# Optimization experiments

Measured on AMD Instinct MI355X. Metric: run time of the kernel, lower is better.

Reference implementation:

```python
import jax, jax.numpy as jnp
import numpy as np

NUM_KP = 17
EDGES = [(0,1),(1,3),(0,2),(2,4),(0,5),(5,7),(7,9),(5,11),(11,13),(13,15),(0,6),(6,8),(8,10),(6,12),(12,14),(14,16)]
NUM_EDGES = len(EDGES)
IMG_H = IMG_W = 401


def bilinear_sampler(x, v):
    # x, v: [N, H, W, 2]. Faithful port of the TF gather_nd bilinear sampler
    # (pad-by-1 border, floor/ceil corners, out-of-bounds -> index 0 into pad).
    N, H, W, C = x.shape
    xp = jnp.pad(x, ((0, 0), (1, 1), (1, 1), (0, 0)))  # zeros pad
    vx = v[..., 0]
    vy = v[..., 1]
    hgrid = jnp.arange(1, H + 1, dtype=jnp.float32)[None, :, None]  # [1,H,1]
    wgrid = jnp.arange(1, W + 1, dtype=jnp.float32)[None, None, :]  # [1,1,W]
    vx0 = jnp.floor(vx); vy0 = jnp.floor(vy)
    vx1 = jnp.ceil(vx);  vy1 = jnp.ceil(vy)
    iy0 = vy0 + hgrid; iy1 = vy1 + hgrid
    ix0 = vx0 + wgrid; ix1 = vx1 + wgrid
    Hf = jnp.float32(H); Wf = jnp.float32(W)
    mask = (ix0 < 1.0) | (iy0 < 1.0) | (ix1 > Wf) | (iy1 > Hf)
    zero = jnp.zeros_like(iy0)
    iy0 = jnp.where(mask, zero, iy0)
    iy1 = jnp.where(mask, zero, iy1)
    ix0 = jnp.where(mask, zero, ix0)
    ix1 = jnp.where(mask, zero, ix1)
    n = jnp.arange(N)[:, None, None]
    iy0i = iy0.astype(jnp.int32); iy1i = iy1.astype(jnp.int32)
    ix0i = ix0.astype(jnp.int32); ix1i = ix1.astype(jnp.int32)
    x00 = xp[n, iy0i, ix0i]  # [N,H,W,C]
    x01 = xp[n, iy1i, ix0i]
    x10 = xp[n, iy0i, ix1i]
    x11 = xp[n, iy1i, ix1i]
    dx = (vx - vx0)[..., None]
    dy = (vy - vy0)[..., None]
    w00 = (1.0 - dx) * (1.0 - dy)
    w01 = (1.0 - dx) * dy
    w10 = dx * (1.0 - dy)
    w11 = dx * dy
    return w00 * x00 + w01 * x01 + w10 * x10 + w11 * x11


def refine(base, offsets, num_steps=2):
    for _ in range(num_steps):
        base = base + bilinear_sampler(offsets, base)
    return base


def conv1x1(x, w, b):
    return jnp.einsum('nhwc,co->nhwo', x, w) + b


def resize(m):
    N, _, _, C = m.shape
    return jax.image.resize(m, (N, IMG_H, IMG_W, C), method='bilinear')


def setup_inputs() -> dict:
    key = jax.random.key(0)
    ks = jax.random.split(key, 11)
    N, H, W, Cin = 2, 13, 13, 2048
    s = 0.01
    return {
        'x': jax.random.normal(ks[0], (N, H, W, Cin), jnp.float32),
        'kp_w': jax.random.normal(ks[1], (Cin, NUM_KP), jnp.float32) * s,
        'kp_b': jax.random.normal(ks[2], (NUM_KP,), jnp.float32) * s,
        'so_w': jax.random.normal(ks[3], (Cin, 2 * NUM_KP), jnp.float32) * s,
        'so_b': jax.random.normal(ks[4], (2 * NUM_KP,), jnp.float32) * s,
        'mo_w': jax.random.normal(ks[5], (Cin, 4 * NUM_EDGES), jnp.float32) * s,
        'mo_b': jax.random.normal(ks[6], (4 * NUM_EDGES,), jnp.float32) * s,
        'lo_w': jax.random.normal(ks[7], (Cin, 2 * NUM_KP), jnp.float32) * s,
        'lo_b': jax.random.normal(ks[8], (2 * NUM_KP,), jnp.float32) * s,
        'ss_w': jax.random.normal(ks[9], (Cin, 1), jnp.float32) * s,
        'ss_b': jax.random.normal(ks[10], (1,), jnp.float32) * s,
    }


def reference(x, kp_w, kp_b, so_w, so_b, mo_w, mo_b, lo_w, lo_b, ss_w, ss_b):
    N = x.shape[0]
    kp = jax.nn.sigmoid(conv1x1(x, kp_w, kp_b))
    so = conv1x1(x, so_w, so_b)
    mo = conv1x1(x, mo_w, mo_b)
    lo = conv1x1(x, lo_w, lo_b)
    ss = jax.nn.sigmoid(conv1x1(x, ss_w, ss_b))
    kp, so, mo, lo, ss = (resize(m) for m in (kp, so, mo, lo, ss))
    # Split channels into (x,y)-offset groups: [K, N, H, W, 2]
    S = so.reshape(N, IMG_H, IMG_W, NUM_KP, 2).transpose(3, 0, 1, 2, 4)
    L = lo.reshape(N, IMG_H, IMG_W, NUM_KP, 2).transpose(3, 0, 1, 2, 4)
    # long: refine against itself, then against short offsets (2 steps each)
    Lr = jax.vmap(lambda l, s: refine(refine(l, l), s))(L, S)
    long_out = Lr.transpose(1, 2, 3, 0, 4).reshape(N, IMG_H, IMG_W, 2 * NUM_KP)
    # mid: one group per directed edge, refined against the target kp short offsets
    n_mid = 2 * NUM_EDGES
    M = mo.reshape(N, IMG_H, IMG_W, n_mid, 2).transpose(3, 0, 1, 2, 4)
    to_kp = jnp.array([e[1] for e in EDGES] + [e[0] for e in EDGES], dtype=jnp.int32)
    Mr = jax.vmap(lambda m, s: refine(m, s))(M, S[to_kp])
    mid_out = Mr.transpose(1, 2, 3, 0, 4).reshape(N, IMG_H, IMG_W, 4 * NUM_EDGES)
    return (kp, so, mid_out, long_out, ss)
```

## Files before the change

kernel.cpp:

```cpp
#include <hip/hip_runtime.h>
#include <math.h>

#define IMG 401
#define NKP 17
#define NMID 32
#define CCH 150

#define OFF_KP   0ULL
#define OFF_SO   5467234ULL
#define OFF_MID  16401702ULL
#define OFF_LONG 36984230ULL
#define OFF_SS   47918698ULL

#define SCc (13.0f/401.0f)
#define C0c (13.0f/802.0f - 0.5f)

typedef float v2f __attribute__((ext_vector_type(2)));

__device__ float  g_coarse[2 * 169 * CCH];
__device__ float2 g_pairs[2 * 66 * 169];

__constant__ int TO_KP_C[32] = {1,3,2,4,5,7,9,11,13,15,6,8,10,12,14,16,
                                0,1,0,2,0,5,7,5,11,13,0,6,8,6,12,14};

__device__ __forceinline__ float med3(float a, float b, float c) {
  return __builtin_amdgcn_fmed3f(a, b, c);
}
__device__ __forceinline__ void store2(float* p, float a, float b) {
  *reinterpret_cast<float2*>(p) = make_float2(a, b);
}
__device__ __forceinline__ v2f ldb(const float2* p, int byteoff) {
  return *reinterpret_cast<const v2f*>(reinterpret_cast<const char*>(p) + byteoff);
}

__global__ __launch_bounds__(512)
void heads_kernel(const float* __restrict__ x,
                  const float* __restrict__ kp_w, const float* __restrict__ kp_b,
                  const float* __restrict__ so_w, const float* __restrict__ so_b,
                  const float* __restrict__ mo_w, const float* __restrict__ mo_b,
                  const float* __restrict__ lo_w, const float* __restrict__ lo_b,
                  const float* __restrict__ ss_w, const float* __restrict__ ss_b) {
  __shared__ float xs[2][2048];
  __shared__ float ps[2][300];
  const int p0 = blockIdx.x * 2;
  const int tid = threadIdx.x;
  const float* xr = x + (size_t)p0 * 2048;
  for (int t = tid; t < 4096; t += 512) xs[t >> 11][t & 2047] = xr[t];
  __syncthreads();
  const int part = tid / 150;
  const int c = tid - part * 150;
  float a0 = 0.f, a1 = 0.f;
  const float* bptr = nullptr; int cc = 0; bool sig = false;
  if (part < 3) {
    const float* wptr; int Ch;
    if (c < 17)       { wptr = kp_w; bptr = kp_b; Ch = 17; cc = c;       sig = true; }
    else if (c < 51)  { wptr = so_w; bptr = so_b; Ch = 34; cc = c - 17; }
    else if (c < 115) { wptr = mo_w; bptr = mo_b; Ch = 64; cc = c - 51; }
    else if (c < 149) { wptr = lo_w; bptr = lo_b; Ch = 34; cc = c - 115; }
    else              { wptr = ss_w; bptr = ss_b; Ch = 1;  cc = 0;       sig = true; }
    const float* wp = wptr + cc;
    const int k0 = part * 683, k1 = (part == 2) ? 2048 : (k0 + 683);
    #pragma unroll 8
    for (int k = k0; k < k1; ++k) {
      float wv = wp[k * Ch];
      a0 = fmaf(xs[0][k], wv, a0);
      a1 = fmaf(xs[1][k], wv, a1);
    }
    if (part) { ps[0][c + (part - 1) * 150] = a0; ps[1][c + (part - 1) * 150] = a1; }
  }
  __syncthreads();
  if (part == 0) {
    float b = bptr[cc];
    float v0 = a0 + ps[0][c] + ps[0][c + 150] + b;
    float v1 = a1 + ps[1][c] + ps[1][c + 150] + b;
    if (sig) { v0 = 1.0f / (1.0f + expf(-v0)); v1 = 1.0f / (1.0f + expf(-v1)); }
    g_coarse[(size_t)p0 * CCH + c] = v0;
    g_coarse[(size_t)(p0 + 1) * CCH + c] = v1;
    if (c >= 17 && c < 149) {
      int rel = c - 17;
      int fi = rel >> 1, lo = rel & 1;
      int nn0 = p0 / 169, pp0 = p0 - nn0 * 169;
      int nn1 = (p0 + 1) / 169, pp1 = (p0 + 1) - nn1 * 169;
      ((float*)g_pairs)[(((size_t)nn0 * 66 + fi) * 169 + pp0) * 2 + lo] = v0;
      ((float*)g_pairs)[(((size_t)nn1 * 66 + fi) * 169 + pp1) * 2 + lo] = v1;
    }
  }
}

struct Pix {
  v2f Q0, Q1;
  v2f SWH;
  v2f LOV;
  v2f HIV;
  int ob;
  int pix;
  bool valid;
};

__device__ __forceinline__ Pix mkpix(int n, int w, int h) {
  Pix P;
  P.valid = (w < IMG) && (h < IMG);
  v2f WH = {(float)w, (float)h};
  v2f S = WH * SCc + C0c;
  float cx = med3(floorf(S.x), 0.f, 11.f);
  float cy = med3(floorf(S.y), 0.f, 11.f);
  float fx = med3(S.x - cx, 0.f, 1.f);
  float fy = med3(S.y - cy, 0.f, 1.f);
  float gx = 1.f - fx, gy = 1.f - fy;
  P.Q0 = (v2f){gx, fx} * gy;
  P.Q1 = (v2f){gx, fx} * fy;
  P.ob = (int)fmaf(cy, 104.f, cx * 8.f);
  P.SWH = S;
  P.LOV = -WH;
  P.HIV = 400.f - WH;
  P.pix = (n * IMG + h) * IMG + w;
  return P;
}

__device__ __forceinline__ v2f blp4b(const float2* __restrict__ F, const Pix& P) {
  return P.Q0.x * ldb(F, P.ob)       + P.Q0.y * ldb(F, P.ob + 8)
       + P.Q1.x * ldb(F, P.ob + 104) + P.Q1.y * ldb(F, P.ob + 112);
}

__device__ __forceinline__ v2f samplePk(const float2* __restrict__ F, v2f v, const Pix& P) {
  v2f F0 = {floorf(v.x), floorf(v.y)};
  v2f D  = v - F0;
  v2f E  = {D.x > 0.f ? 1.f : 0.f, D.y > 0.f ? 1.f : 0.f};
  v2f J1 = F0 + E;
  float sel = (F0.x < P.LOV.x || F0.y < P.LOV.y ||
               J1.x > P.HIV.x || J1.y > P.HIV.y) ? 0.f : 1.f;
  v2f S0 = F0 * SCc + P.SWH;
  v2f S1 = E  * SCc + S0;
  v2f C0 = {med3(floorf(S0.x), 0.f, 11.f), med3(floorf(S0.y), 0.f, 11.f)};
  v2f C1 = {med3(floorf(S1.x), 0.f, 11.f), med3(floorf(S1.y), 0.f, 11.f)};
  v2f U0t = S0 - C0;
  v2f U0 = {med3(U0t.x, 0.f, 1.f), med3(U0t.y, 0.f, 1.f)};
  v2f U1t = S1 - C1;
  v2f U1 = {med3(U1t.x, 0.f, 1.f), med3(U1t.y, 0.f, 1.f)};
  v2f DD = C1 - C0;
  v2f G  = 1.f - D;
  v2f E0 = G * U0;
  v2f E1 = D * U1;
  v2f Fd = D - E1;
  v2f M  = Fd - Fd * DD;
  v2f W0 = (G - E0) + M;
  v2f Tt = Fd - E1;
  v2f W1 = (E0 + E1) + Tt * DD;
  v2f W2 = E1 * DD;
  int a = (int)fmaf(C0.y, 104.f, C0.x * 8.f);
  v2f r0 = W0.x*ldb(F,a)     + W1.x*ldb(F,a+8)   + W2.x*ldb(F,a+16);
  v2f r1 = W0.x*ldb(F,a+104) + W1.x*ldb(F,a+112) + W2.x*ldb(F,a+120);
  v2f r2 = W0.x*ldb(F,a+208) + W1.x*ldb(F,a+216) + W2.x*ldb(F,a+224);
  v2f acc = W0.y*r0 + W1.y*r1 + W2.y*r2;
  return acc * sel;
}

__device__ __forceinline__ void kp_item(int f, int n, int w0, int h0,
                                        const float* __restrict__ cb,
                                        float* __restrict__ out) {
  int r = f / 544, rem = f - r * 544;
  int px = rem / 17, c = rem - px * 17;
  Pix P = mkpix(n, w0 + px, h0 + r);
  if (P.valid) {
    const float* b0 = cb + (P.ob >> 3) * CCH + c;
    float v = P.Q0.x*b0[0] + P.Q0.y*b0[CCH] + P.Q1.x*b0[13*CCH] + P.Q1.y*b0[14*CCH];
    out[OFF_KP + (size_t)P.pix * 17 + c] = v;
  }
}

__device__ __forceinline__ void solong_item(int f, int n, int w0, int h0,
                                            const float2* __restrict__ Sf,
                                            const float2* __restrict__ Lf,
                                            float* __restrict__ out) {
  int r = f / 544, rem = f - r * 544;
  int px = rem / 17, k = rem - px * 17;
  Pix P = mkpix(n, w0 + px, h0 + r);
  const float2* S = Sf + k * 169;
  const float2* L = Lf + k * 169;
  v2f sv = blp4b(S, P);
  v2f b  = blp4b(L, P);
  b += samplePk(L, b, P);
  b += samplePk(L, b, P);
  b += samplePk(S, b, P);
  b += samplePk(S, b, P);
  if (P.valid) {
    store2(out + OFF_SO   + (size_t)P.pix * 34 + 2 * k, sv.x, sv.y);
    store2(out + OFF_LONG + (size_t)P.pix * 34 + 2 * k, b.x, b.y);
  }
}

__device__ __forceinline__ void mid_item(int f, int n, int w0, int h0,
                                         const float2* __restrict__ Sf,
                                         const float2* __restrict__ gmo,
                                         float* __restrict__ out) {
  int r = f >> 10, rem = f & 1023;
  int px = rem >> 5, g = rem & 31;
  Pix P = mkpix(n, w0 + px, h0 + r);
  const float2* G = gmo + g * 169;
  v2f b = blp4b(G, P);
  const float2* S = Sf + TO_KP_C[g] * 169;
  b += samplePk(S, b, P);
  b += samplePk(S, b, P);
  if (P.valid) store2(out + OFF_MID + (size_t)P.pix * 64 + 2 * g, b.x, b.y);
}

__global__ __launch_bounds__(512, 6)
void refine512_kernel(float* __restrict__ out) {
  __shared__ float2 Sf[NKP * 169 + 14];
  __shared__ float2 Lf[NKP * 169 + 14];
  const int n = blockIdx.z;
  const int tid = threadIdx.x;
  const int w0 = blockIdx.x * 32, h0 = blockIdx.y * 16;

  {
    const float2* gS = g_pairs + (size_t)n * 66 * 169;
    const float2* gL = g_pairs + ((size_t)n * 66 + 49) * 169;
    for (int t = tid; t < NKP * 169; t += 512) { Sf[t] = gS[t]; Lf[t] = gL[t]; }
    if (tid < 14) {
      Sf[NKP * 169 + tid] = make_float2(0.f, 0.f);
      Lf[NKP * 169 + tid] = make_float2(0.f, 0.f);
    }
  }
  __syncthreads();

  const float* cb = g_coarse + (size_t)n * 169 * CCH;

  #pragma unroll 1
  for (int it = 0; it < 4; ++it) {
    kp_item(it * 512 + tid, n, w0, h0, cb, out);
    kp_item((it + 4) * 512 + tid, n, w0, h0, cb, out);
    kp_item((it + 8) * 512 + tid, n, w0, h0, cb, out);
    kp_item((it + 12) * 512 + tid, n, w0, h0, cb, out);
  }
  kp_item(16 * 512 + tid, n, w0, h0, cb, out);

  {
    int r = tid >> 5, px = tid & 31;
    Pix P = mkpix(n, w0 + px, h0 + r);
    if (P.valid) {
      const float* b0 = cb + (P.ob >> 3) * CCH + 149;
      out[OFF_SS + (size_t)P.pix] =
          P.Q0.x*b0[0] + P.Q0.y*b0[CCH] + P.Q1.x*b0[13*CCH] + P.Q1.y*b0[14*CCH];
    }
  }

  #pragma unroll 1
  for (int it = 0; it < 5; ++it) {
    solong_item(it * 512 + tid, n, w0, h0, Sf, Lf, out);
    solong_item((it + 5) * 512 + tid, n, w0, h0, Sf, Lf, out);
    solong_item((it + 10) * 512 + tid, n, w0, h0, Sf, Lf, out);
  }
  solong_item(15 * 512 + tid, n, w0, h0, Sf, Lf, out);
  solong_item(16 * 512 + tid, n, w0, h0, Sf, Lf, out);

  const float2* gmo = g_pairs + ((size_t)n * 66 + 17) * 169;
  #pragma unroll 1
  for (int it = 0; it < 8; ++it) {
    mid_item(it * 512 + tid, n, w0, h0, Sf, gmo, out);
    mid_item((it + 8) * 512 + tid, n, w0, h0, Sf, gmo, out);
    mid_item((it + 16) * 512 + tid, n, w0, h0, Sf, gmo, out);
    mid_item((it + 24) * 512 + tid, n, w0, h0, Sf, gmo, out);
  }
}

extern "C" void kernel_launch(void* const* d_in, const int* in_sizes, int n_in,
                              void* d_out, int out_size, void* d_ws, size_t ws_size,
                              hipStream_t stream) {
  const float* x    = (const float*)d_in[0];
  const float* kp_w = (const float*)d_in[1];
  const float* kp_b = (const float*)d_in[2];
  const float* so_w = (const float*)d_in[3];
  const float* so_b = (const float*)d_in[4];
  const float* mo_w = (const float*)d_in[5];
  const float* mo_b = (const float*)d_in[6];
  const float* lo_w = (const float*)d_in[7];
  const float* lo_b = (const float*)d_in[8];
  const float* ss_w = (const float*)d_in[9];
  const float* ss_b = (const float*)d_in[10];
  float* out = (float*)d_out;

  heads_kernel<<<dim3(169), dim3(512), 0, stream>>>(x, kp_w, kp_b, so_w, so_b,
                                                    mo_w, mo_b, lo_w, lo_b,
                                                    ss_w, ss_b);
  refine512_kernel<<<dim3(13, 26, 2), dim3(512), 0, stream>>>(out);
}
```

Baseline: 170.2 us.

## Precompute per-column/row sampling LUTs, shrink tile to 14 rows, interleave two items

Replaces per-item pixel coordinate computation with small shared-memory lookup tables of per-column and per-row bilinear fractions and base offsets, built once per block. Changes the tile height from 16 to 14 rows, which makes the grid 29 rows of blocks and lowers how many pixels past the image edge are wasted. Processes two independent refine chains per thread iteration to expose instruction-level parallelism in the dependent sampler chain. The cost is more registers per thread and extra shared-memory reads, which can lower occupancy.

```diff
diff --git a/kernel.cpp b/kernel.cpp
--- a/kernel.cpp
+++ b/kernel.cpp
@@ -14,6 +14,7 @@
 
 #define SCc (13.0f/401.0f)
 #define C0c (13.0f/802.0f - 0.5f)
+#define ROWS 14
 
 typedef float v2f __attribute__((ext_vector_type(2)));
 
@@ -88,32 +89,25 @@
 }
 
 struct Pix {
-  v2f Q0, Q1;
-  v2f SWH;
-  v2f LOV;
-  v2f HIV;
+  v2f Q0, Q1, SWH, LOV, HIV;
   int ob;
   int pix;
   bool valid;
 };
 
-__device__ __forceinline__ Pix mkpix(int n, int w, int h) {
+__device__ __forceinline__ Pix mkpix2(const float4 lx, const float4 ly,
+                                      int pixbase, int r, int px, int wlim, int hlim) {
   Pix P;
-  P.valid = (w < IMG) && (h < IMG);
-  v2f WH = {(float)w, (float)h};
-  v2f S = WH * SCc + C0c;
-  float cx = med3(floorf(S.x), 0.f, 11.f);
-  float cy = med3(floorf(S.y), 0.f, 11.f);
-  float fx = med3(S.x - cx, 0.f, 1.f);
-  float fy = med3(S.y - cy, 0.f, 1.f);
+  float fx = lx.x, fy = ly.x;
   float gx = 1.f - fx, gy = 1.f - fy;
   P.Q0 = (v2f){gx, fx} * gy;
   P.Q1 = (v2f){gx, fx} * fy;
-  P.ob = (int)fmaf(cy, 104.f, cx * 8.f);
-  P.SWH = S;
-  P.LOV = -WH;
-  P.HIV = 400.f - WH;
-  P.pix = (n * IMG + h) * IMG + w;
+  P.ob  = (int)(lx.z + ly.z);
+  P.SWH = (v2f){lx.y, ly.y};
+  P.LOV = (v2f){-lx.w, -ly.w};
+  P.HIV = (v2f){400.f - lx.w, 400.f - ly.w};
+  P.pix = pixbase + r * IMG + px;
+  P.valid = (px < wlim) && (r < hlim);
   return P;
 }
 
@@ -155,62 +149,17 @@
   return acc * sel;
 }
 
-__device__ __forceinline__ void kp_item(int f, int n, int w0, int h0,
-                                        const float* __restrict__ cb,
-                                        float* __restrict__ out) {
-  int r = f / 544, rem = f - r * 544;
-  int px = rem / 17, c = rem - px * 17;
-  Pix P = mkpix(n, w0 + px, h0 + r);
-  if (P.valid) {
-    const float* b0 = cb + (P.ob >> 3) * CCH + c;
-    float v = P.Q0.x*b0[0] + P.Q0.y*b0[CCH] + P.Q1.x*b0[13*CCH] + P.Q1.y*b0[14*CCH];
-    out[OFF_KP + (size_t)P.pix * 17 + c] = v;
-  }
-}
-
-__device__ __forceinline__ void solong_item(int f, int n, int w0, int h0,
-                                            const float2* __restrict__ Sf,
-                                            const float2* __restrict__ Lf,
-                                            float* __restrict__ out) {
-  int r = f / 544, rem = f - r * 544;
-  int px = rem / 17, k = rem - px * 17;
-  Pix P = mkpix(n, w0 + px, h0 + r);
-  const float2* S = Sf + k * 169;
-  const float2* L = Lf + k * 169;
-  v2f sv = blp4b(S, P);
-  v2f b  = blp4b(L, P);
-  b += samplePk(L, b, P);
-  b += samplePk(L, b, P);
-  b += samplePk(S, b, P);
-  b += samplePk(S, b, P);
-  if (P.valid) {
-    store2(out + OFF_SO   + (size_t)P.pix * 34 + 2 * k, sv.x, sv.y);
-    store2(out + OFF_LONG + (size_t)P.pix * 34 + 2 * k, b.x, b.y);
-  }
-}
-
-__device__ __forceinline__ void mid_item(int f, int n, int w0, int h0,
-                                         const float2* __restrict__ Sf,
-                                         const float2* __restrict__ gmo,
-                                         float* __restrict__ out) {
-  int r = f >> 10, rem = f & 1023;
-  int px = rem >> 5, g = rem & 31;
-  Pix P = mkpix(n, w0 + px, h0 + r);
-  const float2* G = gmo + g * 169;
-  v2f b = blp4b(G, P);
-  const float2* S = Sf + TO_KP_C[g] * 169;
-  b += samplePk(S, b, P);
-  b += samplePk(S, b, P);
-  if (P.valid) store2(out + OFF_MID + (size_t)P.pix * 64 + 2 * g, b.x, b.y);
-}
-
 __global__ __launch_bounds__(512, 6)
 void refine512_kernel(float* __restrict__ out) {
   __shared__ float2 Sf[NKP * 169 + 14];
   __shared__ float2 Lf[NKP * 169 + 14];
+  __shared__ float4 lutX[32];
+  __shared__ float4 lutY[ROWS];
   const int n = blockIdx.z;
   const int tid = threadIdx.x;
-  const int w0 = blockIdx.x * 32, h0 = blockIdx.y * 16;
+  const int w0 = blockIdx.x * 32, h0 = blockIdx.y * ROWS;
+  const int wlim = IMG - w0, hlim = IMG - h0;
+  const int pixbase = (n * IMG + h0) * IMG + w0;
 
   {
     const float2* gS = g_pairs + (size_t)n * 66 * 169;
@@ -219,6 +168,20 @@
     if (tid < 14) {
       Sf[NKP * 169 + tid] = make_float2(0.f, 0.f);
       Lf[NKP * 169 + tid] = make_float2(0.f, 0.f);
+    } else if (tid >= 64 && tid < 96) {
+      int i = tid - 64;
+      float wf = (float)(w0 + i);
+      float S = fmaf(wf, SCc, C0c);
+      float cx = med3(floorf(S), 0.f, 11.f);
+      float fx = med3(S - cx, 0.f, 1.f);
+      lutX[i] = make_float4(fx, S, cx * 8.f, wf);
+    } else if (tid >= 96 && tid < 96 + ROWS) {
+      int j = tid - 96;
+      float hf = (float)(h0 + j);
+      float S = fmaf(hf, SCc, C0c);
+      float cy = med3(floorf(S), 0.f, 11.f);
+      float fy = med3(S - cy, 0.f, 1.f);
+      lutY[j] = make_float4(fy, S, cy * 104.f, hf);
     }
   }
   __syncthreads();
@@ -226,17 +189,22 @@
   const float* cb = g_coarse + (size_t)n * 169 * CCH;
 
   #pragma unroll 1
-  for (int it = 0; it < 4; ++it) {
-    kp_item(it * 512 + tid, n, w0, h0, cb, out);
-    kp_item((it + 4) * 512 + tid, n, w0, h0, cb, out);
-    kp_item((it + 8) * 512 + tid, n, w0, h0, cb, out);
-    kp_item((it + 12) * 512 + tid, n, w0, h0, cb, out);
-  }
-  kp_item(16 * 512 + tid, n, w0, h0, cb, out);
-
-  {
+  for (int it = 0; it < 15; ++it) {
+    int f = it * 512 + tid;
+    if (f >= ROWS * 544) break;
+    int r = f / 544, rem = f - r * 544;
+    int px = rem / 17, c = rem - px * 17;
+    Pix P = mkpix2(lutX[px], lutY[r], pixbase, r, px, wlim, hlim);
+    if (P.valid) {
+      const float* b0 = cb + (P.ob >> 3) * CCH + c;
+      out[OFF_KP + (size_t)P.pix * 17 + c] =
+          P.Q0.x*b0[0] + P.Q0.y*b0[CCH] + P.Q1.x*b0[13*CCH] + P.Q1.y*b0[14*CCH];
+    }
+  }
+
+  if (tid < ROWS * 32) {
     int r = tid >> 5, px = tid & 31;
-    Pix P = mkpix(n, w0 + px, h0 + r);
+    Pix P = mkpix2(lutX[px], lutY[r], pixbase, r, px, wlim, hlim);
     if (P.valid) {
       const float* b0 = cb + (P.ob >> 3) * CCH + 149;
       out[OFF_SS + (size_t)P.pix] =
@@ -245,21 +213,68 @@
   }
 
   #pragma unroll 1
-  for (int it = 0; it < 5; ++it) {
-    solong_item(it * 512 + tid, n, w0, h0, Sf, Lf, out);
-    solong_item((it + 5) * 512 + tid, n, w0, h0, Sf, Lf, out);
-    solong_item((it + 10) * 512 + tid, n, w0, h0, Sf, Lf, out);
-  }
-  solong_item(15 * 512 + tid, n, w0, h0, Sf, Lf, out);
-  solong_item(16 * 512 + tid, n, w0, h0, Sf, Lf, out);
+  for (int it = 0; it < 7; ++it) {
+    int f1 = it * 512 + tid;
+    int f2 = f1 + 3584;
+    int r1 = f1 / 544, rem1 = f1 - r1 * 544, px1 = rem1 / 17, k1 = rem1 - px1 * 17;
+    int r2 = f2 / 544, rem2 = f2 - r2 * 544, px2 = rem2 / 17, k2 = rem2 - px2 * 17;
+    Pix P1 = mkpix2(lutX[px1], lutY[r1], pixbase, r1, px1, wlim, hlim);
+    Pix P2 = mkpix2(lutX[px2], lutY[r2], pixbase, r2, px2, wlim, hlim);
+    const float2* S1 = Sf + k1 * 169; const float2* L1 = Lf + k1 * 169;
+    const float2* S2 = Sf + k2 * 169; const float2* L2 = Lf + k2 * 169;
+    v2f sv1 = blp4b(S1, P1), sv2 = blp4b(S2, P2);
+    v2f b1 = blp4b(L1, P1),  b2 = blp4b(L2, P2);
+    v2f d1, d2;
+    d1 = samplePk(L1, b1, P1); d2 = samplePk(L2, b2, P2); b1 += d1; b2 += d2;
+    d1 = samplePk(L1, b1, P1); d2 = samplePk(L2, b2, P2); b1 += d1; b2 += d2;
+    d1 = samplePk(S1, b1, P1); d2 = samplePk(S2, b2, P2); b1 += d1; b2 += d2;
+    d1 = samplePk(S1, b1, P1); d2 = samplePk(S2, b2, P2); b1 += d1; b2 += d2;
+    if (P1.valid) {
+      store2(out + OFF_SO   + (size_t)P1.pix * 34 + 2 * k1, sv1.x, sv1.y);
+      store2(out + OFF_LONG + (size_t)P1.pix * 34 + 2 * k1, b1.x, b1.y);
+    }
+    if (P2.valid) {
+      store2(out + OFF_SO   + (size_t)P2.pix * 34 + 2 * k2, sv2.x, sv2.y);
+      store2(out + OFF_LONG + (size_t)P2.pix * 34 + 2 * k2, b2.x, b2.y);
+    }
+  }
+  {
+    int f = 3584 * 2 + tid;
+    if (f < ROWS * 544) {
+      int r = f / 544, rem = f - r * 544, px = rem / 17, k = rem - px * 17;
+      Pix P = mkpix2(lutX[px], lutY[r], pixbase, r, px, wlim, hlim);
+      const float2* S = Sf + k * 169; const float2* L = Lf + k * 169;
+      v2f sv = blp4b(S, P);
+      v2f b  = blp4b(L, P);
+      b += samplePk(L, b, P);
+      b += samplePk(L, b, P);
+      b += samplePk(S, b, P);
+      b += samplePk(S, b, P);
+      if (P.valid) {
+        store2(out + OFF_SO   + (size_t)P.pix * 34 + 2 * k, sv.x, sv.y);
+        store2(out + OFF_LONG + (size_t)P.pix * 34 + 2 * k, b.x, b.y);
+      }
+    }
+  }
 
   const float2* gmo = g_pairs + ((size_t)n * 66 + 17) * 169;
   #pragma unroll 1
-  for (int it = 0; it < 8; ++it) {
-    mid_item(it * 512 + tid, n, w0, h0, Sf, gmo, out);
-    mid_item((it + 8) * 512 + tid, n, w0, h0, Sf, gmo, out);
-    mid_item((it + 16) * 512 + tid, n, w0, h0, Sf, gmo, out);
-    mid_item((it + 24) * 512 + tid, n, w0, h0, Sf, gmo, out);
+  for (int it = 0; it < 14; ++it) {
+    int f1 = it * 512 + tid;
+    int f2 = f1 + 7168;
+    int r1 = f1 >> 10, rem1 = f1 & 1023, px1 = rem1 >> 5, g1 = rem1 & 31;
+    int r2 = f2 >> 10, rem2 = f2 & 1023, px2 = rem2 >> 5, g2 = rem2 & 31;
+    Pix P1 = mkpix2(lutX[px1], lutY[r1], pixbase, r1, px1, wlim, hlim);
+    Pix P2 = mkpix2(lutX[px2], lutY[r2], pixbase, r2, px2, wlim, hlim);
+    v2f b1 = blp4b(gmo + g1 * 169, P1);
+    v2f b2 = blp4b(gmo + g2 * 169, P2);
+    const float2* S1 = Sf + TO_KP_C[g1] * 169;
+    const float2* S2 = Sf + TO_KP_C[g2] * 169;
+    v2f d1, d2;
+    d1 = samplePk(S1, b1, P1); d2 = samplePk(S2, b2, P2); b1 += d1; b2 += d2;
+    d1 = samplePk(S1, b1, P1); d2 = samplePk(S2, b2, P2); b1 += d1; b2 += d2;
+    if (P1.valid) store2(out + OFF_MID + (size_t)P1.pix * 64 + 2 * g1, b1.x, b1.y);
+    if (P2.valid) store2(out + OFF_MID + (size_t)P2.pix * 64 + 2 * g2, b2.x, b2.y);
   }
 }
 
@@ -282,5 +297,5 @@
   heads_kernel<<<dim3(169), dim3(512), 0, stream>>>(x, kp_w, kp_b, so_w, so_b,
                                                     mo_w, mo_b, lo_w, lo_b,
                                                     ss_w, ss_b);
-  refine512_kernel<<<dim3(13, 26, 2), dim3(512), 0, stream>>>(out);
-}
+  refine512_kernel<<<dim3(13, 29, 2), dim3(512), 0, stream>>>(out);
+}
```

Measured after the change: 205.7 us. +20.9%, slower.

## Split refine kernel into kp/short/long and mid-offset kernels with separate grids

Applied to the files above, without the earlier changes.

The single fused refine kernel is split into two launches. The first handles keypoint, seg, short and long offsets using 16-row tiles. The second handles the mid offsets with 256-thread blocks on 8-row tiles, and it stages only the short-offset table in LDS. The interleaved unrolled item calls become plain rolled loops. The aim is to cut LDS per block and increase the number of blocks for the mid work, at the cost of an extra launch and recomputing pixel setup.

```diff
diff --git a/kernel.cpp b/kernel.cpp
--- a/kernel.cpp
+++ b/kernel.cpp
@@ -88,10 +88,7 @@
 }
 
 struct Pix {
-  v2f Q0, Q1;
-  v2f SWH;
-  v2f LOV;
-  v2f HIV;
+  v2f Q0, Q1, SWH, LOV, HIV;
   int ob;
   int pix;
   bool valid;
@@ -155,57 +152,8 @@
   return acc * sel;
 }
 
-__device__ __forceinline__ void kp_item(int f, int n, int w0, int h0,
-                                        const float* __restrict__ cb,
-                                        float* __restrict__ out) {
-  int r = f / 544, rem = f - r * 544;
-  int px = rem / 17, c = rem - px * 17;
-  Pix P = mkpix(n, w0 + px, h0 + r);
-  if (P.valid) {
-    const float* b0 = cb + (P.ob >> 3) * CCH + c;
-    float v = P.Q0.x*b0[0] + P.Q0.y*b0[CCH] + P.Q1.x*b0[13*CCH] + P.Q1.y*b0[14*CCH];
-    out[OFF_KP + (size_t)P.pix * 17 + c] = v;
-  }
-}
-
-__device__ __forceinline__ void solong_item(int f, int n, int w0, int h0,
-                                            const float2* __restrict__ Sf,
-                                            const float2* __restrict__ Lf,
-                                            float* __restrict__ out) {
-  int r = f / 544, rem = f - r * 544;
-  int px = rem / 17, k = rem - px * 17;
-  Pix P = mkpix(n, w0 + px, h0 + r);
-  const float2* S = Sf + k * 169;
-  const float2* L = Lf + k * 169;
-  v2f sv = blp4b(S, P);
-  v2f b  = blp4b(L, P);
-  b += samplePk(L, b, P);
-  b += samplePk(L, b, P);
-  b += samplePk(S, b, P);
-  b += samplePk(S, b, P);
-  if (P.valid) {
-    store2(out + OFF_SO   + (size_t)P.pix * 34 + 2 * k, sv.x, sv.y);
-    store2(out + OFF_LONG + (size_t)P.pix * 34 + 2 * k, b.x, b.y);
-  }
-}
-
-__device__ __forceinline__ void mid_item(int f, int n, int w0, int h0,
-                                         const float2* __restrict__ Sf,
-                                         const float2* __restrict__ gmo,
-                                         float* __restrict__ out) {
-  int r = f >> 10, rem = f & 1023;
-  int px = rem >> 5, g = rem & 31;
-  Pix P = mkpix(n, w0 + px, h0 + r);
-  const float2* G = gmo + g * 169;
-  v2f b = blp4b(G, P);
-  const float2* S = Sf + TO_KP_C[g] * 169;
-  b += samplePk(S, b, P);
-  b += samplePk(S, b, P);
-  if (P.valid) store2(out + OFF_MID + (size_t)P.pix * 64 + 2 * g, b.x, b.y);
-}
-
 __global__ __launch_bounds__(512, 6)
-void refine512_kernel(float* __restrict__ out) {
+void refineA_kernel(float* __restrict__ out) {
   __shared__ float2 Sf[NKP * 169 + 14];
   __shared__ float2 Lf[NKP * 169 + 14];
   const int n = blockIdx.z;
@@ -226,13 +174,17 @@
   const float* cb = g_coarse + (size_t)n * 169 * CCH;
 
   #pragma unroll 1
-  for (int it = 0; it < 4; ++it) {
-    kp_item(it * 512 + tid, n, w0, h0, cb, out);
-    kp_item((it + 4) * 512 + tid, n, w0, h0, cb, out);
-    kp_item((it + 8) * 512 + tid, n, w0, h0, cb, out);
-    kp_item((it + 12) * 512 + tid, n, w0, h0, cb, out);
-  }
-  kp_item(16 * 512 + tid, n, w0, h0, cb, out);
+  for (int it = 0; it < 17; ++it) {
+    int f = it * 512 + tid;
+    int r = f / 544, rem = f - r * 544;
+    int px = rem / 17, c = rem - px * 17;
+    Pix P = mkpix(n, w0 + px, h0 + r);
+    if (P.valid) {
+      const float* b0 = cb + (P.ob >> 3) * CCH + c;
+      out[OFF_KP + (size_t)P.pix * 17 + c] =
+          P.Q0.x*b0[0] + P.Q0.y*b0[CCH] + P.Q1.x*b0[13*CCH] + P.Q1.y*b0[14*CCH];
+    }
+  }
 
   {
     int r = tid >> 5, px = tid & 31;
@@ -245,21 +197,53 @@
   }
 
   #pragma unroll 1
-  for (int it = 0; it < 5; ++it) {
-    solong_item(it * 512 + tid, n, w0, h0, Sf, Lf, out);
-    solong_item((it + 5) * 512 + tid, n, w0, h0, Sf, Lf, out);
-    solong_item((it + 10) * 512 + tid, n, w0, h0, Sf, Lf, out);
-  }
-  solong_item(15 * 512 + tid, n, w0, h0, Sf, Lf, out);
-  solong_item(16 * 512 + tid, n, w0, h0, Sf, Lf, out);
+  for (int it = 0; it < 17; ++it) {
+    int f = it * 512 + tid;
+    int r = f / 544, rem = f - r * 544;
+    int px = rem / 17, k = rem - px * 17;
+    Pix P = mkpix(n, w0 + px, h0 + r);
+    const float2* S = Sf + k * 169;
+    const float2* L = Lf + k * 169;
+    v2f sv = blp4b(S, P);
+    v2f b  = blp4b(L, P);
+    b += samplePk(L, b, P);
+    b += samplePk(L, b, P);
+    b += samplePk(S, b, P);
+    b += samplePk(S, b, P);
+    if (P.valid) {
+      store2(out + OFF_SO   + (size_t)P.pix * 34 + 2 * k, sv.x, sv.y);
+      store2(out + OFF_LONG + (size_t)P.pix * 34 + 2 * k, b.x, b.y);
+    }
+  }
+}
+
+__global__ __launch_bounds__(256, 6)
+void refineB_kernel(float* __restrict__ out) {
+  __shared__ float2 Sf[NKP * 169 + 14];
+  const int n = blockIdx.z;
+  const int tid = threadIdx.x;
+  const int w0 = blockIdx.x * 32, h0 = blockIdx.y * 8;
+
+  {
+    const float2* gS = g_pairs + (size_t)n * 66 * 169;
+    for (int t = tid; t < NKP * 169; t += 256) Sf[t] = gS[t];
+    if (tid < 14) Sf[NKP * 169 + tid] = make_float2(0.f, 0.f);
+  }
+  __syncthreads();
 
   const float2* gmo = g_pairs + ((size_t)n * 66 + 17) * 169;
+
   #pragma unroll 1
-  for (int it = 0; it < 8; ++it) {
-    mid_item(it * 512 + tid, n, w0, h0, Sf, gmo, out);
-    mid_item((it + 8) * 512 + tid, n, w0, h0, Sf, gmo, out);
-    mid_item((it + 16) * 512 + tid, n, w0, h0, Sf, gmo, out);
-    mid_item((it + 24) * 512 + tid, n, w0, h0, Sf, gmo, out);
+  for (int it = 0; it < 32; ++it) {
+    int f = it * 256 + tid;
+    int r = f >> 10, rem = f & 1023;
+    int px = rem >> 5, g = rem & 31;
+    Pix P = mkpix(n, w0 + px, h0 + r);
+    v2f b = blp4b(gmo + g * 169, P);
+    const float2* S = Sf + TO_KP_C[g] * 169;
+    b += samplePk(S, b, P);
+    b += samplePk(S, b, P);
+    if (P.valid) store2(out + OFF_MID + (size_t)P.pix * 64 + 2 * g, b.x, b.y);
   }
 }
 
@@ -282,5 +266,6 @@
   heads_kernel<<<dim3(169), dim3(512), 0, stream>>>(x, kp_w, kp_b, so_w, so_b,
                                                     mo_w, mo_b, lo_w, lo_b,
                                                     ss_w, ss_b);
-  refine512_kernel<<<dim3(13, 26, 2), dim3(512), 0, stream>>>(out);
-}
+  refineA_kernel<<<dim3(13, 26, 2), dim3(512), 0, stream>>>(out);
+  refineB_kernel<<<dim3(13, 51, 2), dim3(256), 0, stream>>>(out);
+}
```

Result: slower. 179.2 us (+5.3%).
